# Performance work log

Measured on AMD Instinct MI355X. Metric: run time of the kernel, lower is better.

## Reference

```python
import jax, jax.numpy as jnp
import numpy as np

B, S, D, H, L = 8, 4096, 512, 512, 2


def log_g(x):
    # log of g(x) where g(x) = x + 0.5 for x >= 0 else sigmoid(x)
    return jnp.where(x >= 0, jnp.log(jax.nn.relu(x) + 0.5), -jax.nn.softplus(-x))


def g(x):
    return jnp.where(x >= 0, x + 0.5, jax.nn.sigmoid(x))


def mingru_layer(x, h0, wz, bz, wh, bh):
    """Log-space parallel-scan minGRU layer.
    x: (B,S,Din), h0: (B,1,H) positive (already g-activated).
    wz,wh: (H,Din); bz,bh: (H,). Returns full hidden sequence (B,S,H)."""
    k = jnp.einsum('bsd,hd->bsh', x, wz) + bz          # gate pre-activation
    log_z = -jax.nn.softplus(-k)                        # log sigmoid(k)
    log_coeffs = -jax.nn.softplus(k)                    # log(1 - sigmoid(k))
    log_h_tilde = log_g(jnp.einsum('bsd,hd->bsh', x, wh) + bh)
    log_values = log_z + log_h_tilde                    # log(z * h_tilde)
    log_h0 = jnp.log(h0)                                # (B,1,H)
    # Heinsen associative scan in log space
    a_star = jnp.cumsum(
        jnp.concatenate([jnp.zeros_like(log_h0), log_coeffs], axis=1), axis=1)  # (B,S+1,H)
    log_vals = jnp.concatenate([log_h0, log_values], axis=1)                     # (B,S+1,H)
    log_h = a_star + jax.lax.cumlogsumexp(log_vals - a_star, axis=1)
    return jnp.exp(log_h)[:, 1:]                        # (B,S,H)


def setup_inputs() -> dict:
    key = jax.random.key(0)
    ks = jax.random.split(key, 1 + 4 * L)
    x = jax.random.normal(ks[0], (B, S, D), dtype=jnp.float32)
    inp = {'x': x}
    dims_in = [D] + [H] * (L - 1)
    i = 1
    for l in range(L):
        din = dims_in[l]
        stdv = 1.0 / np.sqrt(din)
        inp[f'wz{l}'] = jax.random.uniform(ks[i], (H, din), minval=-stdv, maxval=stdv); i += 1
        inp[f'bz{l}'] = jax.random.uniform(ks[i], (H,), minval=-stdv, maxval=stdv); i += 1
        inp[f'wh{l}'] = jax.random.uniform(ks[i], (H, din), minval=-stdv, maxval=stdv); i += 1
        inp[f'bh{l}'] = jax.random.uniform(ks[i], (H,), minval=-stdv, maxval=stdv); i += 1
    return inp


def reference(x, wz0, bz0, wh0, bh0, wz1, bz1, wh1, bh1):
    # h is None -> h0 = g(zeros) = 0.5 for every layer
    h0 = jnp.full((B, 1, H), 0.5, dtype=x.dtype)
    params = [(wz0, bz0, wh0, bh0), (wz1, bz1, wh1, bh1)]
    inp = x
    finals = []
    for (wz, bz, wh, bh) in params:
        out = mingru_layer(inp, h0, wz, bz, wh, bh)
        finals.append(out[:, -1:])
        inp = out  # Identity layer transform, no residual, dropout=0
    return out, jnp.stack(finals)  # (B,S,H), (L,B,1,H)
```

## Files before the change

kernel.cpp:

```cpp
#include <hip/hip_runtime.h>
#include <math.h>

#define BB 8
#define SS 4096
#define DD 512
#define HH 512
#define MM (BB*SS)

constexpr int TCH = 64;
constexpr int NC  = SS / TCH;
constexpr int BH  = BB * HH;

constexpr int BM = 128;
constexpr int BN = 64;
constexpr int BK = 64;

typedef short  short8  __attribute__((ext_vector_type(8)));
typedef float  float4v __attribute__((ext_vector_type(4)));
typedef float  float2v __attribute__((ext_vector_type(2)));

__device__ inline unsigned short f2bf(float f) {
    union { float f; unsigned u; } v; v.f = f;
    unsigned r = v.u + 0x7FFF + ((v.u >> 16) & 1);
    return (unsigned short)(r >> 16);
}
__device__ inline float bf_lo(unsigned u) {
    union { unsigned u; float f; } x; x.u = u << 16; return x.f;
}
__device__ inline float bf_hi(unsigned u) {
    union { unsigned u; float f; } x; x.u = u & 0xffff0000u; return x.f;
}
__device__ inline float fast_rcp(float x) {
    return __builtin_amdgcn_rcpf(x);
}

__device__ inline void async_copy16(const void* g, void* l) {
    __builtin_amdgcn_global_load_lds(
        (const __attribute__((address_space(1))) void*)g,
        (__attribute__((address_space(3))) void*)l, 16, 0, 0);
}

__global__ __launch_bounds__(256)
void conv_all(const float* __restrict__ x,
              const float* __restrict__ w0, const float* __restrict__ w1,
              const float* __restrict__ w2, const float* __restrict__ w3,
              short* __restrict__ Xbf, short* __restrict__ Wbf)
{
    constexpr int XBLK = MM * DD / 8 / 256;
    constexpr int WBLK = HH * DD / 8 / 256;
    const int bid = blockIdx.x;
    const float* src; short* dst; size_t base;
    if (bid < XBLK) {
        src = x; dst = Xbf;
        base = ((size_t)bid * 256 + threadIdx.x) * 8;
    } else {
        const int idx  = bid - XBLK;
        const int wsel = idx / WBLK;
        src = (wsel == 0) ? w0 : (wsel == 1) ? w1 : (wsel == 2) ? w2 : w3;
        dst = Wbf + (size_t)wsel * HH * DD;
        base = ((size_t)(idx % WBLK) * 256 + threadIdx.x) * 8;
    }
    float4 a = *(const float4*)(src + base);
    float4 b = *(const float4*)(src + base + 4);
    short8 r;
    r[0] = f2bf(a.x); r[1] = f2bf(a.y); r[2] = f2bf(a.z); r[3] = f2bf(a.w);
    r[4] = f2bf(b.x); r[5] = f2bf(b.y); r[6] = f2bf(b.z); r[7] = f2bf(b.w);
    *(short8*)(dst + base) = r;
}

__global__ __launch_bounds__(256)
void gemm_gate_mfma(const short* __restrict__ Xg, const short* __restrict__ Wz,
                    const float* __restrict__ bz, const short* __restrict__ Wh,
                    const float* __restrict__ bh, unsigned* __restrict__ AV,
                    float2* __restrict__ cAV)
{
    __shared__ char smem[65536];
    short* lds = (short*)smem;
    constexpr int BUFS = 16384;
    constexpr int ZOFF = BM * BK;
    constexpr int HOFF = ZOFF + BN * BK;
    constexpr int NIT  = DD / BK;

    const int t    = threadIdx.x;
    const int wave = t >> 6;
    const int lane = t & 63;
    const int col16 = lane & 15;
    const int quad  = lane >> 4;
    const int wm = wave >> 1;
    const int wn = wave & 1;
    const int m0 = blockIdx.x * BM;
    const int n0 = blockIdx.y * BN;

    float4v accz[4][2], acch[4][2];
    #pragma unroll
    for (int i = 0; i < 4; ++i)
        #pragma unroll
        for (int j = 0; j < 2; ++j) {
            accz[i][j] = (float4v){0.f, 0.f, 0.f, 0.f};
            acch[i][j] = (float4v){0.f, 0.f, 0.f, 0.f};
        }

    const int lr  = lane >> 3;
    const int lcs = (((lane & 7) ^ lr) * 8);

    auto stage = [&](int buf, int k0) {
        short* L = lds + buf * BUFS;
        #pragma unroll
        for (int i = 0; i < 4; ++i) {
            const int r0 = wave * 32 + i * 8;
            async_copy16(Xg + (size_t)(m0 + r0 + lr) * DD + k0 + lcs,
                         &L[r0 * BK]);
        }
        #pragma unroll
        for (int i = 0; i < 2; ++i) {
            const int r0 = wave * 16 + i * 8;
            async_copy16(Wz + (size_t)(n0 + r0 + lr) * DD + k0 + lcs,
                         &L[ZOFF + r0 * BK]);
            async_copy16(Wh + (size_t)(n0 + r0 + lr) * DD + k0 + lcs,
                         &L[HOFF + r0 * BK]);
        }
    };

    stage(0, 0);
    asm volatile("s_waitcnt vmcnt(0)" ::: "memory");
    __builtin_amdgcn_s_barrier();
    asm volatile("" ::: "memory");

    const int swz = (col16 & 7) * 8;

    #pragma unroll
    for (int it = 0; it < NIT; ++it) {
        if (it + 1 < NIT) stage((it + 1) & 1, (it + 1) * BK);

        const short* L = lds + (it & 1) * BUFS;
        #pragma unroll
        for (int kk = 0; kk < 2; ++kk) {
            const int ko = (kk * 32 + quad * 8) ^ swz;
            short8 af[4], bzf[2], bhf[2];
            #pragma unroll
            for (int mi = 0; mi < 4; ++mi)
                af[mi] = *(const short8*)&L[(wm*64 + mi*16 + col16) * BK + ko];
            #pragma unroll
            for (int nj = 0; nj < 2; ++nj) {
                bzf[nj] = *(const short8*)&L[ZOFF + (wn*32 + nj*16 + col16) * BK + ko];
                bhf[nj] = *(const short8*)&L[HOFF + (wn*32 + nj*16 + col16) * BK + ko];
            }
            #pragma unroll
            for (int mi = 0; mi < 4; ++mi)
                #pragma unroll
                for (int nj = 0; nj < 2; ++nj) {
                    accz[mi][nj] = __builtin_amdgcn_mfma_f32_16x16x32_bf16(af[mi], bzf[nj], accz[mi][nj], 0, 0, 0);
                    acch[mi][nj] = __builtin_amdgcn_mfma_f32_16x16x32_bf16(af[mi], bhf[nj], acch[mi][nj], 0, 0, 0);
                }
        }
        asm volatile("s_waitcnt vmcnt(0) lgkmcnt(0)" ::: "memory");
        __builtin_amdgcn_s_barrier();
        asm volatile("" ::: "memory");
    }

    {
        const int b  = m0 >> 12;
        const int cw = ((m0 & 4095) >> 6) + wm;

        #pragma unroll
        for (int nj = 0; nj < 2; ++nj) {
            const int ln = wn*32 + nj*16 + col16;
            const int n  = n0 + ln;
            const float bzn = bz[n], bhn = bh[n];
            float cA = 1.0f, cV = 0.0f;
            #pragma unroll
            for (int mi = 0; mi < 4; ++mi) {
                float sA = 1.0f, sV = 0.0f;
                const size_t mbase = (size_t)(m0 + wm*64 + mi*16 + quad*4) * HH + n;
                #pragma unroll
                for (int reg = 0; reg < 4; ++reg) {
                    const float kz = accz[mi][nj][reg] + bzn;
                    const float kh = acch[mi][nj][reg] + bhn;
                    const float a  = fast_rcp(1.0f + __expf(kz));
                    const float sn = fast_rcp(1.0f + __expf(-kh));
                    const float ht = (kh >= 0.0f) ? (kh + 0.5f) : sn;
                    const float v  = (1.0f - a) * ht;
                    const unsigned u = ((unsigned)f2bf(v) << 16) | f2bf(a);
                    AV[mbase + (size_t)reg * HH] = u;
                    const float ar = bf_lo(u), vr = bf_hi(u);
                    sV = fmaf(ar, sV, vr);
                    sA *= ar;
                }
                {
                    float oA = __shfl_xor(sA, 16), oV = __shfl_xor(sV, 16);
                    float lA = (quad & 1) ? oA : sA, lV = (quad & 1) ? oV : sV;
                    float rA = (quad & 1) ? sA : oA, rV = (quad & 1) ? sV : oV;
                    sA = lA * rA; sV = fmaf(rA, lV, rV);
                    oA = __shfl_xor(sA, 32); oV = __shfl_xor(sV, 32);
                    lA = (quad & 2) ? oA : sA; lV = (quad & 2) ? oV : sV;
                    rA = (quad & 2) ? sA : oA; rV = (quad & 2) ? sV : oV;
                    sA = lA * rA; sV = fmaf(rA, lV, rV);
                }
                cV = fmaf(sA, cV, sV);
                cA = cA * sA;
            }
            if (quad == 0)
                cAV[(size_t)cw * BH + b * HH + n] = make_float2(cA, cV);
        }
    }
}

__global__ __launch_bounds__(256)
void scan_apply_f32(const unsigned* __restrict__ AV,
                    const float2* __restrict__ cAV,
                    float* __restrict__ out, float* __restrict__ finals)
{
    const int h  = 2 * threadIdx.x;
    const int b  = blockIdx.y;
    const int c  = blockIdx.z;
    const int ch = b * HH + h;
    float h0c = 0.5f, h1c = 0.5f;
    for (int cp = 0; cp < c; ++cp) {
        const float4 s = *(const float4*)&cAV[(size_t)cp * BH + ch];
        h0c = fmaf(s.x, h0c, s.y);
        h1c = fmaf(s.z, h1c, s.w);
    }
    size_t base = ((size_t)(b * SS + c * TCH)) * HH + h;
    #pragma unroll
    for (int tt = 0; tt < TCH; ++tt) {
        const uint2 u = *(const uint2*)&AV[base];
        h0c = fmaf(bf_lo(u.x), h0c, bf_hi(u.x));
        h1c = fmaf(bf_lo(u.y), h1c, bf_hi(u.y));
        float2v o; o[0] = h0c; o[1] = h1c;
        __builtin_nontemporal_store(o, (float2v*)&out[base]);
        base += HH;
    }
    if (c == NC - 1) {
        float2v f; f[0] = h0c; f[1] = h1c;
        *(float2v*)&finals[ch] = f;
    }
}

__global__ __launch_bounds__(256)
void scan_apply_bf16(const unsigned* __restrict__ AV,
                     const float2* __restrict__ cAV,
                     short* __restrict__ out, float* __restrict__ finals)
{
    const int h  = 2 * threadIdx.x;
    const int b  = blockIdx.y;
    const int c  = blockIdx.z;
    const int ch = b * HH + h;
    float h0c = 0.5f, h1c = 0.5f;
    for (int cp = 0; cp < c; ++cp) {
        const float4 s = *(const float4*)&cAV[(size_t)cp * BH + ch];
        h0c = fmaf(s.x, h0c, s.y);
        h1c = fmaf(s.z, h1c, s.w);
    }
    size_t base = ((size_t)(b * SS + c * TCH)) * HH + h;
    #pragma unroll
    for (int tt = 0; tt < TCH; ++tt) {
        const uint2 u = *(const uint2*)&AV[base];
        h0c = fmaf(bf_lo(u.x), h0c, bf_hi(u.x));
        h1c = fmaf(bf_lo(u.y), h1c, bf_hi(u.y));
        *(unsigned*)&out[base] = (unsigned)f2bf(h0c) | ((unsigned)f2bf(h1c) << 16);
        base += HH;
    }
    if (c == NC - 1) {
        float2v f; f[0] = h0c; f[1] = h1c;
        *(float2v*)&finals[ch] = f;
    }
}

extern "C" void kernel_launch(void* const* d_in, const int* in_sizes, int n_in,
                              void* d_out, int out_size, void* d_ws, size_t ws_size,
                              hipStream_t stream)
{
    const float* x   = (const float*)d_in[0];
    const float* wz0 = (const float*)d_in[1];
    const float* bz0 = (const float*)d_in[2];
    const float* wh0 = (const float*)d_in[3];
    const float* bh0 = (const float*)d_in[4];
    const float* wz1 = (const float*)d_in[5];
    const float* bz1 = (const float*)d_in[6];
    const float* wh1 = (const float*)d_in[7];
    const float* bh1 = (const float*)d_in[8];

    float* out    = (float*)d_out;
    float* finals = out + (size_t)MM * HH;

    unsigned* AV  = (unsigned*)d_ws;
    short* Xbf    = (short*)(AV + (size_t)MM * HH);
    short* Wbf    = Xbf + (size_t)MM * DD;
    float2* cAV   = (float2*)(Wbf + (size_t)4 * HH * DD);

    short* Wz0 = Wbf;
    short* Wh0 = Wbf + (size_t)1 * HH * DD;
    short* Wz1 = Wbf + (size_t)2 * HH * DD;
    short* Wh1 = Wbf + (size_t)3 * HH * DD;

    const dim3 gg(MM / BM, HH / BN);
    const dim3 gs(1, BB, NC);

    conv_all<<<MM * DD / 8 / 256 + 4 * (HH * DD / 8 / 256), 256, 0, stream>>>(
        x, wz0, wh0, wz1, wh1, Xbf, Wbf);

    gemm_gate_mfma <<<gg, 256, 0, stream>>>(Xbf, Wz0, bz0, Wh0, bh0, AV, cAV);
    scan_apply_bf16<<<gs, 256, 0, stream>>>(AV, cAV, Xbf, finals);

    gemm_gate_mfma <<<gg, 256, 0, stream>>>(Xbf, Wz1, bz1, Wh1, bh1, AV, cAV);
    scan_apply_f32 <<<gs, 256, 0, stream>>>(AV, cAV, out, finals + BH);
}
```

Before: 303.0 us.

## Fuse fp32-to-bf16 conversion into GEMM staging and drop separate convert kernel

Removes the standalone conv_all kernel. The GEMM now loads fp32 x and weights into registers, converts them to bf16 and writes them to LDS itself, with the register load issued before the MFMA loop so it overlaps compute. This avoids one kernel launch and the full write and re-read of the bf16 copy of x, which is the largest buffer. In exchange, the first GEMM reads twice as many bytes for x, re-converts the weights in every block, and uses more registers. Launch bounds are also set to 2 blocks per CU.

```diff
diff --git a/kernel.cpp b/kernel.cpp
--- a/kernel.cpp
+++ b/kernel.cpp
@@ -40,39 +40,21 @@
         (__attribute__((address_space(3))) void*)l, 16, 0, 0);
 }
 
-__global__ __launch_bounds__(256)
-void conv_all(const float* __restrict__ x,
-              const float* __restrict__ w0, const float* __restrict__ w1,
-              const float* __restrict__ w2, const float* __restrict__ w3,
-              short* __restrict__ Xbf, short* __restrict__ Wbf)
-{
-    constexpr int XBLK = MM * DD / 8 / 256;
-    constexpr int WBLK = HH * DD / 8 / 256;
-    const int bid = blockIdx.x;
-    const float* src; short* dst; size_t base;
-    if (bid < XBLK) {
-        src = x; dst = Xbf;
-        base = ((size_t)bid * 256 + threadIdx.x) * 8;
-    } else {
-        const int idx  = bid - XBLK;
-        const int wsel = idx / WBLK;
-        src = (wsel == 0) ? w0 : (wsel == 1) ? w1 : (wsel == 2) ? w2 : w3;
-        dst = Wbf + (size_t)wsel * HH * DD;
-        base = ((size_t)(idx % WBLK) * 256 + threadIdx.x) * 8;
-    }
-    float4 a = *(const float4*)(src + base);
-    float4 b = *(const float4*)(src + base + 4);
+__device__ inline short8 cvt8(const float4 a, const float4 b) {
     short8 r;
-    r[0] = f2bf(a.x); r[1] = f2bf(a.y); r[2] = f2bf(a.z); r[3] = f2bf(a.w);
-    r[4] = f2bf(b.x); r[5] = f2bf(b.y); r[6] = f2bf(b.z); r[7] = f2bf(b.w);
-    *(short8*)(dst + base) = r;
-}
-
-__global__ __launch_bounds__(256)
-void gemm_gate_mfma(const short* __restrict__ Xg, const short* __restrict__ Wz,
-                    const float* __restrict__ bz, const short* __restrict__ Wh,
-                    const float* __restrict__ bh, unsigned* __restrict__ AV,
-                    float2* __restrict__ cAV)
+    r[0] = (short)f2bf(a.x); r[1] = (short)f2bf(a.y);
+    r[2] = (short)f2bf(a.z); r[3] = (short)f2bf(a.w);
+    r[4] = (short)f2bf(b.x); r[5] = (short)f2bf(b.y);
+    r[6] = (short)f2bf(b.z); r[7] = (short)f2bf(b.w);
+    return r;
+}
+
+template<bool XF32>
+__global__ __launch_bounds__(256, 2)
+void gemm_gate_mfma(const void* __restrict__ Xsrc,
+                    const float* __restrict__ Wz, const float* __restrict__ bz,
+                    const float* __restrict__ Wh, const float* __restrict__ bh,
+                    unsigned* __restrict__ AV, float2* __restrict__ cAV)
 {
     __shared__ char smem[65536];
     short* lds = (short*)smem;
@@ -91,6 +73,9 @@
     const int m0 = blockIdx.x * BM;
     const int n0 = blockIdx.y * BN;
 
+    const short* Xg16 = (const short*)Xsrc;
+    const float* Xg32 = (const float*)Xsrc;
+
     float4v accz[4][2], acch[4][2];
     #pragma unroll
     for (int i = 0; i < 4; ++i)
@@ -103,26 +88,61 @@
     const int lr  = lane >> 3;
     const int lcs = (((lane & 7) ^ lr) * 8);
 
-    auto stage = [&](int buf, int k0) {
+    float4 xr[4][2];
+    float4 wzr[2][2], whr[2][2];
+
+    auto stageX_lds = [&](int buf, int k0) {
         short* L = lds + buf * BUFS;
         #pragma unroll
         for (int i = 0; i < 4; ++i) {
             const int r0 = wave * 32 + i * 8;
-            async_copy16(Xg + (size_t)(m0 + r0 + lr) * DD + k0 + lcs,
+            async_copy16(Xg16 + (size_t)(m0 + r0 + lr) * DD + k0 + lcs,
                          &L[r0 * BK]);
         }
+    };
+    auto stageX_issue = [&](int k0) {
+        #pragma unroll
+        for (int i = 0; i < 4; ++i) {
+            const int r0 = wave * 32 + i * 8;
+            const float* p = Xg32 + (size_t)(m0 + r0 + lr) * DD + k0 + lcs;
+            xr[i][0] = *(const float4*)p;
+            xr[i][1] = *(const float4*)(p + 4);
+        }
+    };
+    auto stageX_write = [&](int buf) {
+        short* L = lds + buf * BUFS;
+        #pragma unroll
+        for (int i = 0; i < 4; ++i) {
+            const int r0 = wave * 32 + i * 8;
+            *(short8*)&L[r0 * BK + lane * 8] = cvt8(xr[i][0], xr[i][1]);
+        }
+    };
+    auto stageW_issue = [&](int k0) {
         #pragma unroll
         for (int i = 0; i < 2; ++i) {
             const int r0 = wave * 16 + i * 8;
-            async_copy16(Wz + (size_t)(n0 + r0 + lr) * DD + k0 + lcs,
-                         &L[ZOFF + r0 * BK]);
-            async_copy16(Wh + (size_t)(n0 + r0 + lr) * DD + k0 + lcs,
-                         &L[HOFF + r0 * BK]);
-        }
-    };
-
-    stage(0, 0);
+            const float* pz = Wz + (size_t)(n0 + r0 + lr) * DD + k0 + lcs;
+            const float* ph = Wh + (size_t)(n0 + r0 + lr) * DD + k0 + lcs;
+            wzr[i][0] = *(const float4*)pz; wzr[i][1] = *(const float4*)(pz + 4);
+            whr[i][0] = *(const float4*)ph; whr[i][1] = *(const float4*)(ph + 4);
+        }
+    };
+    auto stageW_write = [&](int buf) {
+        short* L = lds + buf * BUFS;
+        #pragma unroll
+        for (int i = 0; i < 2; ++i) {
+            const int r0 = wave * 16 + i * 8;
+            *(short8*)&L[ZOFF + r0 * BK + lane * 8] = cvt8(wzr[i][0], wzr[i][1]);
+            *(short8*)&L[HOFF + r0 * BK + lane * 8] = cvt8(whr[i][0], whr[i][1]);
+        }
+    };
+
+    if constexpr (XF32) stageX_issue(0); else stageX_lds(0, 0);
+    stageW_issue(0);
     asm volatile("s_waitcnt vmcnt(0)" ::: "memory");
+    if constexpr (XF32) stageX_write(0);
+    stageW_write(0);
+    asm volatile("s_waitcnt lgkmcnt(0)" ::: "memory");
     __builtin_amdgcn_s_barrier();
     asm volatile("" ::: "memory");
 
@@ -130,7 +150,12 @@
 
     #pragma unroll
     for (int it = 0; it < NIT; ++it) {
-        if (it + 1 < NIT) stage((it + 1) & 1, (it + 1) * BK);
+        if (it + 1 < NIT) {
+            if constexpr (XF32) stageX_issue((it + 1) * BK);
+            else                stageX_lds((it + 1) & 1, (it + 1) * BK);
+            stageW_issue((it + 1) * BK);
+        }
+        asm volatile("" ::: "memory");
 
         const short* L = lds + (it & 1) * BUFS;
         #pragma unroll
@@ -153,7 +178,12 @@
                     acch[mi][nj] = __builtin_amdgcn_mfma_f32_16x16x32_bf16(af[mi], bhf[nj], acch[mi][nj], 0, 0, 0);
                 }
         }
-        asm volatile("s_waitcnt vmcnt(0) lgkmcnt(0)" ::: "memory");
+        asm volatile("s_waitcnt vmcnt(0)" ::: "memory");
+        if (it + 1 < NIT) {
+            if constexpr (XF32) stageX_write((it + 1) & 1);
+            stageW_write((it + 1) & 1);
+        }
+        asm volatile("s_waitcnt lgkmcnt(0)" ::: "memory");
         __builtin_amdgcn_s_barrier();
         asm volatile("" ::: "memory");
     }
@@ -285,23 +315,14 @@
 
     unsigned* AV  = (unsigned*)d_ws;
     short* Xbf    = (short*)(AV + (size_t)MM * HH);
-    short* Wbf    = Xbf + (size_t)MM * DD;
-    float2* cAV   = (float2*)(Wbf + (size_t)4 * HH * DD);
-
-    short* Wz0 = Wbf;
-    short* Wh0 = Wbf + (size_t)1 * HH * DD;
-    short* Wz1 = Wbf + (size_t)2 * HH * DD;
-    short* Wh1 = Wbf + (size_t)3 * HH * DD;
+    float2* cAV   = (float2*)(Xbf + (size_t)MM * HH);
 
     const dim3 gg(MM / BM, HH / BN);
     const dim3 gs(1, BB, NC);
 
-    conv_all<<<MM * DD / 8 / 256 + 4 * (HH * DD / 8 / 256), 256, 0, stream>>>(
-        x, wz0, wh0, wz1, wh1, Xbf, Wbf);
-
-    gemm_gate_mfma <<<gg, 256, 0, stream>>>(Xbf, Wz0, bz0, Wh0, bh0, AV, cAV);
-    scan_apply_bf16<<<gs, 256, 0, stream>>>(AV, cAV, Xbf, finals);
-
-    gemm_gate_mfma <<<gg, 256, 0, stream>>>(Xbf, Wz1, bz1, Wh1, bh1, AV, cAV);
-    scan_apply_f32 <<<gs, 256, 0, stream>>>(AV, cAV, out, finals + BH);
-}
+    gemm_gate_mfma<true> <<<gg, 256, 0, stream>>>(x,   wz0, bz0, wh0, bh0, AV, cAV);
+    scan_apply_bf16      <<<gs, 256, 0, stream>>>(AV, cAV, Xbf, finals);
+
+    gemm_gate_mfma<false><<<gg, 256, 0, stream>>>(Xbf, wz1, bz1, wh1, bh1, AV, cAV);
+    scan_apply_f32       <<<gs, 256, 0, stream>>>(AV, cAV, out, finals + BH);
+}
```

Result: slower. 358.2 us (+18.2%).
